# Optimization experiments

Measured on AMD Instinct MI355X. Metric: run time of the kernel, lower is better.

## Reference

```python
import jax, jax.numpy as jnp
import numpy as np
from jax import lax

MODES = 16
DEPTH = 8
NPH = 8  # photons = sum(init_state); init_state = [1]*8 + [0]*8
IDX = np.arange(NPH)  # output_indices derived from init_state
PI = np.pi
CHUNK = 4096  # pairs per permanent chunk (memory control, mirrors chunk_subsets idea)


def setup_inputs() -> dict:
    key = jax.random.key(0)
    k1, k2, k3 = jax.random.split(key, 3)
    x = jax.random.normal(k1, (256, 64), dtype=jnp.float32)
    W = jax.random.normal(k2, (120, 64), dtype=jnp.float32) / np.sqrt(64.0)
    b = jax.random.normal(k3, (120,), dtype=jnp.float32) * 0.01
    return {"x": x, "W": W, "b": b}


def _forward(x, W, b):
    N = x.shape[0]
    # fc1 + sigmoid embedding -> angle pairs
    x_emb = jax.nn.sigmoid(x @ W.T + b)              # (N, 120)
    tbu = x_emb.reshape(N, -1, 2)                    # (N, T, 2)
    theta = tbu[:, :, 0] * (PI / 2)
    phi = tbu[:, :, 1] * (2 * PI)
    ct = jnp.cos(theta).astype(jnp.complex64)
    st = jnp.sin(theta).astype(jnp.complex64)
    ep = jnp.exp(1j * phi.astype(jnp.complex64))
    # 2x2 tunable beam-splitter unitaries: [[e^{i phi} c, -s], [e^{i phi} s, c]]
    row0 = jnp.stack([ep * ct, -st], axis=-1)
    row1 = jnp.stack([ep * st, ct], axis=-1)
    blocks = jnp.stack([row0, row1], axis=-2)        # (N, T, 2, 2)

    # Apply block-diagonal layers. Block-diag matmul only mixes row pairs,
    # so update row segments directly instead of building (modes,modes) UBS.
    U = jnp.broadcast_to(jnp.eye(MODES, dtype=jnp.complex64), (N, MODES, MODES))
    nb_even, nb_odd = MODES // 2, (MODES - 2) // 2
    n_before = 0
    for d in range(DEPTH):
        if d % 2 == 0:
            nb, off = nb_even, 0
        else:
            nb, off = nb_odd, 1
        blk = blocks[:, n_before:n_before + nb]                      # (N, nb, 2, 2)
        seg = U[:, off:off + 2 * nb, :].reshape(N, nb, 2, MODES)     # row pairs
        new = jnp.einsum('nkab,nkbm->nkam', blk, seg).reshape(N, 2 * nb, MODES)
        U = U.at[:, off:off + 2 * nb, :].set(new)
        n_before += nb

    # Photonic Gram: K[a,b] = |perm( (U_a^dag U_b)[idx, idx] )|^2.
    # Only the idx-columns of U enter: V = U[:, :, idx], submatrix = V_a^dag V_b.
    V = U[:, :, IDX]                                  # (N, MODES, n)
    G = jnp.einsum('ami,bmj->abij', V.conj(), V)      # (N, N, n, n)

    n = NPH
    subsets = jnp.arange(1, 1 << n)                   # (S,), S = 2^n - 1
    masks = (subsets[:, None] >> jnp.arange(n)[None, :]) & 1   # (S, n)
    signs = (1 - 2 * ((n - masks.sum(axis=1)) & 1)).astype(jnp.complex64)
    maskc = masks.astype(jnp.complex64)

    A = G.reshape(N * N, n, n)
    nc = (N * N) // CHUNK

    def perm_chunk(Ac):  # Ryser: sum_S (-1)^{n-|S|} prod_i sum_{j in S} A_ij
        ss = jnp.einsum('cij,sj->csi', Ac, maskc)     # (c, S, n) subset row-sums
        pr = jnp.prod(ss, axis=2)                     # (c, S)
        return jnp.sum(pr * signs, axis=1)            # (c,)

    perms = lax.map(perm_chunk, A.reshape(nc, CHUNK, n, n)).reshape(N * N)
    K = (jnp.abs(perms) ** 2).astype(jnp.float32).reshape(N, N)
    di = jnp.arange(N)
    K = K.at[di, di].set(1.0)
    return x_emb, K


def reference(x, W, b):
    return _forward(x, W, b)
```

## Files before the change

### kernel.cpp

```cpp
#include <hip/hip_runtime.h>
#include <math.h>

#define NS 256
#define EMB 120
#define NBLK 60
#define MODES 16
#define NPH 8

typedef float v2f __attribute__((ext_vector_type(2)));

__device__ __forceinline__ v2f cmul(v2f a, v2f b) {
    v2f axx = {a.x, a.x};
    v2f nyy = {-a.y, a.y};
    v2f byx = {b.y, b.x};
    return axx * b + nyy * byx;
}
__device__ __forceinline__ v2f cfma_conj(v2f a, v2f b, v2f c) {
    v2f axx = {a.x, a.x};
    v2f pyy = {a.y, -a.y};
    v2f byx = {b.y, b.x};
    return axx * b + (pyy * byx + c);
}

__device__ __forceinline__ float dpp_xor1(float x) {
    return __builtin_bit_cast(float,
        __builtin_amdgcn_mov_dpp(__builtin_bit_cast(int, x), 0xB1, 0xF, 0xF, true));
}
__device__ __forceinline__ float dpp_xor2(float x) {
    return __builtin_bit_cast(float,
        __builtin_amdgcn_mov_dpp(__builtin_bit_cast(int, x), 0x4E, 0xF, 0xF, true));
}

__global__ __launch_bounds__(128) void emb_v_kernel(
    const float* __restrict__ x, const float* __restrict__ W,
    const float* __restrict__ bias, float* __restrict__ out_emb,
    float2* __restrict__ Vws)
{
    const int s = blockIdx.x;
    const int t = threadIdx.x;
    __shared__ float emb[EMB];
    __shared__ float ctA[NBLK], stA[NBLK], exA[NBLK], eyA[NBLK];

    if (t < EMB) {
        const float* xr = x + s * 64;
        const float* wr = W + t * 64;
        float acc = bias[t];
        #pragma unroll
        for (int k = 0; k < 64; ++k) acc = fmaf(xr[k], wr[k], acc);
        float e = 1.0f / (1.0f + expf(-acc));
        emb[t] = e;
        out_emb[s * EMB + t] = e;
    }
    __syncthreads();

    if (t < NBLK) {
        float th = emb[2 * t]     * 1.57079632679489662f;
        float ph = emb[2 * t + 1] * 6.28318530717958648f;
        float st, ct, sp, cp;
        sincosf(th, &st, &ct);
        sincosf(ph, &sp, &cp);
        ctA[t] = ct; stA[t] = st; exA[t] = cp; eyA[t] = sp;
    }
    __syncthreads();

    if (t < NPH) {
        const int c = t;
        float2 u[MODES];
        #pragma unroll
        for (int m = 0; m < MODES; ++m) {
            u[m].x = (m == c) ? 1.0f : 0.0f;
            u[m].y = 0.0f;
        }
        int bi = 0;
        #pragma unroll
        for (int d = 0; d < 8; ++d) {
            const int off = d & 1;
            const int nb = 8 - off;
            #pragma unroll
            for (int k = 0; k < nb; ++k) {
                float ct = ctA[bi], st = stA[bi], ex = exA[bi], ey = eyA[bi];
                ++bi;
                const int r0 = off + 2 * k;
                float2 u0 = u[r0], u1 = u[r0 + 1];
                float2 n0, n1;
                n0.x = ex * ct * u0.x - ey * ct * u0.y - st * u1.x;
                n0.y = ex * ct * u0.y + ey * ct * u0.x - st * u1.y;
                n1.x = ex * st * u0.x - ey * st * u0.y + ct * u1.x;
                n1.y = ex * st * u0.y + ey * st * u0.x + ct * u1.y;
                u[r0] = n0; u[r0 + 1] = n1;
            }
        }
        #pragma unroll
        for (int m = 0; m < MODES; ++m)
            Vws[(s * MODES + m) * NPH + c] = u[m];
    }
}

__global__ __launch_bounds__(256, 2) void perm_kernel(
    const float2* __restrict__ Vws, float* __restrict__ outK)
{
    __shared__ float2 sva[8][132];
    __shared__ float2 svb[8][132];

    const int L = blockIdx.x;
    int t = (int)((65.0f - sqrtf(4225.0f - 8.0f * (float)L)) * 0.5f);
    while (t * (65 - t) / 2 > L) --t;
    while ((t + 1) * (65 - (t + 1)) / 2 <= L) ++t;
    const int ta = t;
    const int tb = ta + (L - t * (65 - t) / 2);

    const int tid = threadIdx.x;
    const float4* srcA = (const float4*)(Vws + (size_t)ta * 8 * 128);
    const float4* srcB = (const float4*)(Vws + (size_t)tb * 8 * 128);
    #pragma unroll
    for (int r = 0; r < 2; ++r) {
        int idx = r * 256 + tid;
        int row = idx >> 6;
        int c4  = idx & 63;
        *(float4*)&sva[row][c4 * 2] = srcA[idx];
        *(float4*)&svb[row][c4 * 2] = srcB[idx];
    }
    __syncthreads();

    const int p   = tid >> 2;
    const int sub = tid & 3;
    const int h   = sub & 1;
    const int e   = sub >> 1;
    const int pa  = p >> 3;
    const int pb  = p & 7;

    v2f Go[2][8];
    #pragma unroll
    for (int i = 0; i < 2; ++i)
        #pragma unroll
        for (int j = 0; j < 8; ++j) Go[i][j] = (v2f){0.f, 0.f};

    #pragma unroll 2
    for (int m = 0; m < 16; ++m) {
        float4 va4 = *(const float4*)&sva[pa][m * 8 + 4 * h + 2 * e];
        v2f a0 = {va4.x, va4.y};
        v2f a1 = {va4.z, va4.w};
        v2f vb[8];
        #pragma unroll
        for (int jj = 0; jj < 4; ++jj) {
            float4 b4 = *(const float4*)&svb[pb][m * 8 + 2 * jj];
            vb[2 * jj]     = (v2f){b4.x, b4.y};
            vb[2 * jj + 1] = (v2f){b4.z, b4.w};
        }
        #pragma unroll
        for (int j = 0; j < 8; ++j) {
            Go[0][j] = cfma_conj(a0, vb[j], Go[0][j]);
            Go[1][j] = cfma_conj(a1, vb[j], Go[1][j]);
        }
    }

    v2f Gp[2][8];
    #pragma unroll
    for (int i = 0; i < 2; ++i)
        #pragma unroll
        for (int j = 0; j < 8; ++j) {
            Gp[i][j].x = dpp_xor2(Go[i][j].x);
            Gp[i][j].y = dpp_xor2(Go[i][j].y);
        }

    const float sgn = 1.0f - 2.0f * (float)e;
    const v2f sgnv = {sgn, sgn};
    v2f rs[4];
    #pragma unroll
    for (int r = 0; r < 2; ++r) {
        {
            v2f s = ((Go[r][0] + Go[r][1]) + (Go[r][2] + Go[r][3]))
                  + ((Go[r][4] + Go[r][5]) + Go[r][6]);
            rs[r] = sgnv * Go[r][7] + s;
        }
        {
            v2f s = ((Gp[r][0] + Gp[r][1]) + (Gp[r][2] + Gp[r][3]))
                  + ((Gp[r][4] + Gp[r][5]) + Gp[r][6]);
            rs[2 + r] = sgnv * Gp[r][7] + s;
        }
    }

    v2f acc;

#define TREE(OUT) do {                                                \
        v2f t01 = cmul(rs[0], rs[1]);                                 \
        v2f t23 = cmul(rs[2], rs[3]);                                 \
        v2f half = cmul(t01, t23);                                    \
        v2f oth;                                                      \
        oth.x = dpp_xor1(half.x);                                     \
        oth.y = dpp_xor1(half.y);                                     \
        OUT = cmul(half, oth);                                        \
    } while (0)

#define UPD(J, S) do {                                                \
        const v2f sv = {(S), (S)};                                    \
        rs[0] = sv * Go[0][J] + rs[0];                                \
        rs[1] = sv * Go[1][J] + rs[1];                                \
        rs[2] = sv * Gp[0][J] + rs[2];                                \
        rs[3] = sv * Gp[1][J] + rs[3];                                \
    } while (0)

#define TERM(TS) do {                                                 \
        v2f fullp; TREE(fullp);                                       \
        const v2f tv = {(TS), (TS)};                                  \
        acc = tv * fullp + acc;                                       \
    } while (0)

    TREE(acc);
    UPD(1, -2.f); TERM(-1.f);
    UPD(2, -2.f); TERM( 1.f);
    UPD(1,  2.f); TERM(-1.f);
    UPD(3, -2.f); TERM( 1.f);
    UPD(1, -2.f); TERM(-1.f);
    UPD(2,  2.f); TERM( 1.f);
    UPD(1,  2.f); TERM(-1.f);
    UPD(4, -2.f); TERM( 1.f);
    UPD(1, -2.f); TERM(-1.f);
    UPD(2, -2.f); TERM( 1.f);
    UPD(1,  2.f); TERM(-1.f);
    UPD(3,  2.f); TERM( 1.f);
    UPD(1, -2.f); TERM(-1.f);
    UPD(2,  2.f); TERM( 1.f);
    UPD(1,  2.f); TERM(-1.f);
    UPD(5, -2.f); TERM( 1.f);
    UPD(1, -2.f); TERM(-1.f);
    UPD(2, -2.f); TERM( 1.f);
    UPD(1,  2.f); TERM(-1.f);
    UPD(3, -2.f); TERM( 1.f);
    UPD(1, -2.f); TERM(-1.f);
    UPD(2,  2.f); TERM( 1.f);
    UPD(1,  2.f); TERM(-1.f);
    UPD(4,  2.f); TERM( 1.f);
    UPD(1, -2.f); TERM(-1.f);
    UPD(2, -2.f); TERM( 1.f);
    UPD(1,  2.f); TERM(-1.f);
    UPD(3,  2.f); TERM( 1.f);
    UPD(1, -2.f); TERM(-1.f);
    UPD(2,  2.f); TERM( 1.f);
    UPD(1,  2.f); TERM(-1.f);
    UPD(6, -2.f); TERM( 1.f);
    UPD(1, -2.f); TERM(-1.f);
    UPD(2, -2.f); TERM( 1.f);
    UPD(1,  2.f); TERM(-1.f);
    UPD(3, -2.f); TERM( 1.f);
    UPD(1, -2.f); TERM(-1.f);
    UPD(2,  2.f); TERM( 1.f);
    UPD(1,  2.f); TERM(-1.f);
    UPD(4, -2.f); TERM( 1.f);
    UPD(1, -2.f); TERM(-1.f);
    UPD(2, -2.f); TERM( 1.f);
    UPD(1,  2.f); TERM(-1.f);
    UPD(3,  2.f); TERM( 1.f);
    UPD(1, -2.f); TERM(-1.f);
    UPD(2,  2.f); TERM( 1.f);
    UPD(1,  2.f); TERM(-1.f);
    UPD(5,  2.f); TERM( 1.f);
    UPD(1, -2.f); TERM(-1.f);
    UPD(2, -2.f); TERM( 1.f);
    UPD(1,  2.f); TERM(-1.f);
    UPD(3, -2.f); TERM( 1.f);
    UPD(1, -2.f); TERM(-1.f);
    UPD(2,  2.f); TERM( 1.f);
    UPD(1,  2.f); TERM(-1.f);
    UPD(4,  2.f); TERM( 1.f);
    UPD(1, -2.f); TERM(-1.f);
    UPD(2, -2.f); TERM( 1.f);
    UPD(1,  2.f); TERM(-1.f);
    UPD(3,  2.f); TERM( 1.f);
    UPD(1, -2.f); TERM(-1.f);
    UPD(2,  2.f); TERM( 1.f);
    UPD(1,  2.f); TERM(-1.f);
#undef UPD
#undef TERM
#undef TREE

    float ax = sgn * acc.x, ay = sgn * acc.y;
    ax += dpp_xor2(ax);
    ay += dpp_xor2(ay);

    if (sub == 0) {
        const int a = ta * 8 + pa;
        const int b = tb * 8 + pb;
        float K = fmaf(ax, ax, ay * ay) * (1.0f / 16384.0f);
        if (a == b) K = 1.0f;
        outK[a * 256 + b] = K;
        outK[b * 256 + a] = K;
    }
}

extern "C" void kernel_launch(void* const* d_in, const int* in_sizes, int n_in,
                              void* d_out, int out_size, void* d_ws, size_t ws_size,
                              hipStream_t stream) {
    const float* x    = (const float*)d_in[0];
    const float* W    = (const float*)d_in[1];
    const float* bias = (const float*)d_in[2];
    float* out     = (float*)d_out;
    float* out_emb = out;
    float* outK    = out + NS * EMB;
    float2* Vws    = (float2*)d_ws;

    emb_v_kernel<<<NS, 128, 0, stream>>>(x, W, bias, out_emb, Vws);
    perm_kernel<<<528, 256, 0, stream>>>(Vws, outK);
}
```

Measured before the change: 75.59 us.

## Fuse embedding and unitary construction into permanent kernel with per-block recompute

```diff
diff --git a/kernel.cpp b/kernel.cpp
--- a/kernel.cpp
+++ b/kernel.cpp
@@ -3,7 +3,6 @@
 
 #define NS 256
 #define EMB 120
-#define NBLK 60
 #define MODES 16
 #define NPH 8
 
@@ -31,40 +30,82 @@
         __builtin_amdgcn_mov_dpp(__builtin_bit_cast(int, x), 0x4E, 0xF, 0xF, true));
 }
 
-__global__ __launch_bounds__(128) void emb_v_kernel(
+__global__ __launch_bounds__(256, 2) void fused_perm_kernel(
     const float* __restrict__ x, const float* __restrict__ W,
     const float* __restrict__ bias, float* __restrict__ out_emb,
-    float2* __restrict__ Vws)
+    float* __restrict__ outK)
 {
-    const int s = blockIdx.x;
-    const int t = threadIdx.x;
-    __shared__ float emb[EMB];
-    __shared__ float ctA[NBLK], stA[NBLK], exA[NBLK], eyA[NBLK];
-
-    if (t < EMB) {
-        const float* xr = x + s * 64;
-        const float* wr = W + t * 64;
-        float acc = bias[t];
-        #pragma unroll
-        for (int k = 0; k < 64; ++k) acc = fmaf(xr[k], wr[k], acc);
-        float e = 1.0f / (1.0f + expf(-acc));
-        emb[t] = e;
-        out_emb[s * EMB + t] = e;
+    __shared__ __align__(16) float2 sva[8][132];
+    __shared__ __align__(16) float2 svb[8][132];
+    __shared__ __align__(16) float  xls[16][64];
+    __shared__ float  embl[16][120];
+    __shared__ __align__(16) float  angl[16][61][4];
+
+    const int L = blockIdx.x;
+    int t = (int)((65.0f - sqrtf(4225.0f - 8.0f * (float)L)) * 0.5f);
+    while (t * (65 - t) / 2 > L) --t;
+    while ((t + 1) * (65 - (t + 1)) / 2 <= L) ++t;
+    const int ta = t;
+    const int tb = ta + (L - t * (65 - t) / 2);
+
+    const int tid = threadIdx.x;
+
+    {
+        const int i  = tid >> 4;
+        const int q  = tid & 15;
+        const int si = (i < 8) ? (ta * 8 + i) : (tb * 8 + (i - 8));
+        const float4 xv = ((const float4*)(x + (size_t)si * 64))[q];
+        *(float4*)&xls[i][q * 4] = xv;
     }
     __syncthreads();
 
-    if (t < NBLK) {
-        float th = emb[2 * t]     * 1.57079632679489662f;
-        float ph = emb[2 * t + 1] * 6.28318530717958648f;
-        float st, ct, sp, cp;
-        sincosf(th, &st, &ct);
-        sincosf(ph, &sp, &cp);
-        ctA[t] = ct; stA[t] = st; exA[t] = cp; eyA[t] = sp;
+    {
+        const int i  = tid >> 4;
+        const int jb = tid & 15;
+        const float4* W4 = (const float4*)W;
+        #pragma unroll
+        for (int r = 0; r < 8; ++r) {
+            const int j = jb + 16 * r;
+            if (j < EMB) {
+                float acc = bias[j];
+                const float4* wr = W4 + j * 16;
+                #pragma unroll
+                for (int k4 = 0; k4 < 16; ++k4) {
+                    const float4 w = wr[k4];
+                    acc = fmaf(xls[i][k4 * 4 + 0], w.x, acc);
+                    acc = fmaf(xls[i][k4 * 4 + 1], w.y, acc);
+                    acc = fmaf(xls[i][k4 * 4 + 2], w.z, acc);
+                    acc = fmaf(xls[i][k4 * 4 + 3], w.w, acc);
+                }
+                const float e = 1.0f / (1.0f + expf(-acc));
+                embl[i][j] = e;
+                if (ta == tb && i < 8)
+                    out_emb[(size_t)(ta * 8 + i) * EMB + j] = e;
+            }
+        }
     }
     __syncthreads();
 
-    if (t < NPH) {
-        const int c = t;
+    #pragma unroll
+    for (int r = 0; r < 4; ++r) {
+        const int idx = tid + 256 * r;
+        if (idx < 960) {
+            const int i = idx / 60;
+            const int b = idx - i * 60;
+            const float th = embl[i][2 * b]     * 1.57079632679489662f;
+            const float ph = embl[i][2 * b + 1] * 6.28318530717958648f;
+            float st, ct, sp, cp;
+            sincosf(th, &st, &ct);
+            sincosf(ph, &sp, &cp);
+            angl[i][b][0] = ct; angl[i][b][1] = st;
+            angl[i][b][2] = cp; angl[i][b][3] = sp;
+        }
+    }
+    __syncthreads();
+
+    if (tid < 128) {
+        const int i = tid >> 3;
+        const int c = tid & 7;
         float2 u[MODES];
         #pragma unroll
         for (int m = 0; m < MODES; ++m) {
@@ -78,7 +119,8 @@
             const int nb = 8 - off;
             #pragma unroll
             for (int k = 0; k < nb; ++k) {
-                float ct = ctA[bi], st = stA[bi], ex = exA[bi], ey = eyA[bi];
+                const float4 a4 = *(const float4*)&angl[i][bi][0];
+                const float ct = a4.x, st = a4.y, ex = a4.z, ey = a4.w;
                 ++bi;
                 const int r0 = off + 2 * k;
                 float2 u0 = u[r0], u1 = u[r0 + 1];
@@ -90,35 +132,10 @@
                 u[r0] = n0; u[r0 + 1] = n1;
             }
         }
+        float2* dst = (i < 8) ? &sva[i][0] : &svb[i - 8][0];
         #pragma unroll
         for (int m = 0; m < MODES; ++m)
-            Vws[(s * MODES + m) * NPH + c] = u[m];
-    }
-}
-
-__global__ __launch_bounds__(256, 2) void perm_kernel(
-    const float2* __restrict__ Vws, float* __restrict__ outK)
-{
-    __shared__ float2 sva[8][132];
-    __shared__ float2 svb[8][132];
-
-    const int L = blockIdx.x;
-    int t = (int)((65.0f - sqrtf(4225.0f - 8.0f * (float)L)) * 0.5f);
-    while (t * (65 - t) / 2 > L) --t;
-    while ((t + 1) * (65 - (t + 1)) / 2 <= L) ++t;
-    const int ta = t;
-    const int tb = ta + (L - t * (65 - t) / 2);
-
-    const int tid = threadIdx.x;
-    const float4* srcA = (const float4*)(Vws + (size_t)ta * 8 * 128);
-    const float4* srcB = (const float4*)(Vws + (size_t)tb * 8 * 128);
-    #pragma unroll
-    for (int r = 0; r < 2; ++r) {
-        int idx = r * 256 + tid;
-        int row = idx >> 6;
-        int c4  = idx & 63;
-        *(float4*)&sva[row][c4 * 2] = srcA[idx];
-        *(float4*)&svb[row][c4 * 2] = srcB[idx];
+            dst[m * 8 + c] = u[m];
     }
     __syncthreads();
 
@@ -297,8 +314,7 @@
     float* out     = (float*)d_out;
     float* out_emb = out;
     float* outK    = out + NS * EMB;
-    float2* Vws    = (float2*)d_ws;
-
-    emb_v_kernel<<<NS, 128, 0, stream>>>(x, W, bias, out_emb, Vws);
-    perm_kernel<<<528, 256, 0, stream>>>(Vws, outK);
-}
+    (void)d_ws; (void)ws_size; (void)in_sizes; (void)n_in;
+
+    fused_perm_kernel<<<528, 256, 0, stream>>>(x, W, bias, out_emb, outK);
+}
```

New measurement: 111.1 us. 47.0% more time.

## Split permanent Gray-code walk across eight lanes and double block count

Applied to the files above, without the earlier changes.

```diff
diff --git a/kernel.cpp b/kernel.cpp
--- a/kernel.cpp
+++ b/kernel.cpp
@@ -29,6 +29,10 @@
 __device__ __forceinline__ float dpp_xor2(float x) {
     return __builtin_bit_cast(float,
         __builtin_amdgcn_mov_dpp(__builtin_bit_cast(int, x), 0x4E, 0xF, 0xF, true));
+}
+__device__ __forceinline__ float swz_xor4(float x) {
+    return __builtin_bit_cast(float,
+        __builtin_amdgcn_ds_swizzle(__builtin_bit_cast(int, x), 0x101F));
 }
 
 __global__ __launch_bounds__(128) void emb_v_kernel(
@@ -96,13 +100,14 @@
     }
 }
 
-__global__ __launch_bounds__(256, 2) void perm_kernel(
+__global__ __launch_bounds__(256, 4) void perm_kernel(
     const float2* __restrict__ Vws, float* __restrict__ outK)
 {
     __shared__ float2 sva[8][132];
     __shared__ float2 svb[8][132];
 
-    const int L = blockIdx.x;
+    const int L  = blockIdx.x >> 1;
+    const int hb = blockIdx.x & 1;
     int t = (int)((65.0f - sqrtf(4225.0f - 8.0f * (float)L)) * 0.5f);
     while (t * (65 - t) / 2 > L) --t;
     while ((t + 1) * (65 - (t + 1)) / 2 <= L) ++t;
@@ -122,11 +127,12 @@
     }
     __syncthreads();
 
-    const int p   = tid >> 2;
-    const int sub = tid & 3;
+    const int p   = tid >> 3;
+    const int sub = tid & 7;
     const int h   = sub & 1;
-    const int e   = sub >> 1;
-    const int pa  = p >> 3;
+    const int e   = (sub >> 1) & 1;
+    const int f   = sub >> 2;
+    const int pa  = (hb << 2) | (p >> 3);
     const int pb  = p & 7;
 
     v2f Go[2][8];
@@ -163,20 +169,24 @@
             Gp[i][j].y = dpp_xor2(Go[i][j].y);
         }
 
-    const float sgn = 1.0f - 2.0f * (float)e;
-    const v2f sgnv = {sgn, sgn};
+    const float sgne = 1.0f - 2.0f * (float)e;
+    const float sgnf = 1.0f - 2.0f * (float)f;
+    const v2f sev = {sgne, sgne};
+    const v2f sfv = {sgnf, sgnf};
     v2f rs[4];
     #pragma unroll
     for (int r = 0; r < 2; ++r) {
         {
             v2f s = ((Go[r][0] + Go[r][1]) + (Go[r][2] + Go[r][3]))
-                  + ((Go[r][4] + Go[r][5]) + Go[r][6]);
-            rs[r] = sgnv * Go[r][7] + s;
+                  + (Go[r][4] + Go[r][5]);
+            s = sfv * Go[r][6] + s;
+            rs[r] = sev * Go[r][7] + s;
         }
         {
             v2f s = ((Gp[r][0] + Gp[r][1]) + (Gp[r][2] + Gp[r][3]))
-                  + ((Gp[r][4] + Gp[r][5]) + Gp[r][6]);
-            rs[2 + r] = sgnv * Gp[r][7] + s;
+                  + (Gp[r][4] + Gp[r][5]);
+            s = sfv * Gp[r][6] + s;
+            rs[2 + r] = sev * Gp[r][7] + s;
         }
     }
 
@@ -185,11 +195,11 @@
 #define TREE(OUT) do {                                                \
         v2f t01 = cmul(rs[0], rs[1]);                                 \
         v2f t23 = cmul(rs[2], rs[3]);                                 \
-        v2f half = cmul(t01, t23);                                    \
+        v2f half_ = cmul(t01, t23);                                   \
         v2f oth;                                                      \
-        oth.x = dpp_xor1(half.x);                                     \
-        oth.y = dpp_xor1(half.y);                                     \
-        OUT = cmul(half, oth);                                        \
+        oth.x = dpp_xor1(half_.x);                                    \
+        oth.y = dpp_xor1(half_.y);                                    \
+        OUT = cmul(half_, oth);                                       \
     } while (0)
 
 #define UPD(J, S) do {                                                \
@@ -238,45 +248,16 @@
     UPD(1, -2.f); TERM(-1.f);
     UPD(2,  2.f); TERM( 1.f);
     UPD(1,  2.f); TERM(-1.f);
-    UPD(6, -2.f); TERM( 1.f);
-    UPD(1, -2.f); TERM(-1.f);
-    UPD(2, -2.f); TERM( 1.f);
-    UPD(1,  2.f); TERM(-1.f);
-    UPD(3, -2.f); TERM( 1.f);
-    UPD(1, -2.f); TERM(-1.f);
-    UPD(2,  2.f); TERM( 1.f);
-    UPD(1,  2.f); TERM(-1.f);
-    UPD(4, -2.f); TERM( 1.f);
-    UPD(1, -2.f); TERM(-1.f);
-    UPD(2, -2.f); TERM( 1.f);
-    UPD(1,  2.f); TERM(-1.f);
-    UPD(3,  2.f); TERM( 1.f);
-    UPD(1, -2.f); TERM(-1.f);
-    UPD(2,  2.f); TERM( 1.f);
-    UPD(1,  2.f); TERM(-1.f);
-    UPD(5,  2.f); TERM( 1.f);
-    UPD(1, -2.f); TERM(-1.f);
-    UPD(2, -2.f); TERM( 1.f);
-    UPD(1,  2.f); TERM(-1.f);
-    UPD(3, -2.f); TERM( 1.f);
-    UPD(1, -2.f); TERM(-1.f);
-    UPD(2,  2.f); TERM( 1.f);
-    UPD(1,  2.f); TERM(-1.f);
-    UPD(4,  2.f); TERM( 1.f);
-    UPD(1, -2.f); TERM(-1.f);
-    UPD(2, -2.f); TERM( 1.f);
-    UPD(1,  2.f); TERM(-1.f);
-    UPD(3,  2.f); TERM( 1.f);
-    UPD(1, -2.f); TERM(-1.f);
-    UPD(2,  2.f); TERM( 1.f);
-    UPD(1,  2.f); TERM(-1.f);
 #undef UPD
 #undef TERM
 #undef TREE
 
-    float ax = sgn * acc.x, ay = sgn * acc.y;
+    const float cf = sgne * sgnf;
+    float ax = cf * acc.x, ay = cf * acc.y;
     ax += dpp_xor2(ax);
     ay += dpp_xor2(ay);
+    ax += swz_xor4(ax);
+    ay += swz_xor4(ay);
 
     if (sub == 0) {
         const int a = ta * 8 + pa;
@@ -300,5 +281,5 @@
     float2* Vws    = (float2*)d_ws;
 
     emb_v_kernel<<<NS, 128, 0, stream>>>(x, W, bias, out_emb, Vws);
-    perm_kernel<<<528, 256, 0, stream>>>(Vws, outK);
-}
+    perm_kernel<<<1056, 256, 0, stream>>>(Vws, outK);
+}
```

Result: slower. 77.64 us (+2.7%).
